# Kernel tuning notes

Hardware: AMD Instinct MI355X
Metric: run time of the kernel (lower is better)

The kernel has to match this reference:

```python
import jax, jax.numpy as jnp
import numpy as np

OUT = 260        # RESIZE_OUTPUT_IMAGES_SHAPE
TH = 0.8         # OD_SCORE_TH
PCT = 1.0        # INTERNAL_PERCENTAGE_IMAGE_TOTAKE
N_BOXES = 10     # loop bound in original call()
TAPS = 6         # lanczos3 support (radius 3 -> 6 taps, antialias=False)


def _lanczos_taps(src, size):
    """src: (OUT,) float sample coords in crop-local space; size: traced int crop size.
    Returns clamped tap indices (OUT,6) and normalized lanczos3 weights (OUT,6)."""
    base = jnp.floor(src).astype(jnp.int32) - 2
    taps = base[:, None] + jnp.arange(TAPS, dtype=jnp.int32)          # (OUT,6)
    d = src[:, None] - taps.astype(src.dtype)
    w = jnp.where(jnp.abs(d) < 3.0, jnp.sinc(d) * jnp.sinc(d / 3.0), 0.0)
    w = w / jnp.sum(w, axis=1, keepdims=True)
    idx = jnp.clip(taps, 0, size - 1)
    return idx, w


def _crop_resize(img, box):
    """img: (H,W,3). box: (4,) normalized [ymin,xmin,ymax,xmax] -> (OUT,OUT,3).
    Matches tf.image.resize lanczos3 (antialias=False): half-pixel centers, clamped edges."""
    H, W = img.shape[0], img.shape[1]
    y0 = (box[0] * H).astype(jnp.int32)
    x0 = (box[1] * W).astype(jnp.int32)
    y1 = (box[2] * H).astype(jnp.int32)
    x1 = (box[3] * W).astype(jnp.int32)
    ch = jnp.maximum(y1 - y0, 1)
    cw = jnp.maximum(x1 - x0, 1)
    o = jnp.arange(OUT, dtype=img.dtype)
    src_h = (o + 0.5) * (ch.astype(img.dtype) / OUT) - 0.5
    src_w = (o + 0.5) * (cw.astype(img.dtype) / OUT) - 0.5
    idx_h, w_h = _lanczos_taps(src_h, ch)
    idx_w, w_w = _lanczos_taps(src_w, cw)
    idx_h = idx_h + y0
    idx_w = idx_w + x0
    # vertical pass: gather 6 row taps per output row, reduce -> (OUT, W, 3)
    rows = jnp.einsum('pa,pawc->pwc', w_h, img[idx_h])
    # horizontal pass: gather 6 col taps per output col, reduce -> (OUT, OUT, 3)
    out = jnp.einsum('qb,pqbc->pqc', w_w, rows[:, idx_w])
    return out


def setup_inputs() -> dict:
    key = jax.random.key(0)
    k1, k2, k3, k4 = jax.random.split(key, 4)
    # scores: first 10 mostly above threshold, rest below
    s_hi = 0.85 + 0.15 * jax.random.uniform(k1, (N_BOXES,), dtype=jnp.float32)
    s_lo = 0.8 * jax.random.uniform(k2, (100 - N_BOXES,), dtype=jnp.float32)
    od_scores = jnp.concatenate([s_hi, s_lo])
    # bboxes (ymin,xmin,ymax,xmax) with guaranteed positive crop sizes
    u = jax.random.uniform(k3, (100, 4), dtype=jnp.float32)
    od_bboxes = jnp.stack([u[:, 0] * 0.45, u[:, 1] * 0.45,
                           0.55 + 0.45 * u[:, 2], 0.55 + 0.45 * u[:, 3]], axis=1)
    image = jax.random.normal(k4, (1, 2048, 2048, 3), dtype=jnp.float32)
    return {"od_scores": od_scores, "od_bboxes": od_bboxes, "image": image}


def reference(od_scores, od_bboxes, image):
    img = image[0]                           # (H,W,3)
    b10 = od_bboxes[:N_BOXES]
    s10 = od_scores[:N_BOXES]
    valid = ((od_scores[0] >= TH) & (s10 >= TH)
             & (b10[:, 1] >= 0.5 - PCT / 2.0)
             & (b10[:, 3] <= 0.5 + PCT / 2.0))
    crops = jax.vmap(lambda b: _crop_resize(img, b))(b10)   # (10,OUT,OUT,3)
    return crops * valid[:, None, None, None].astype(img.dtype)
```

## Files before the change

kernel.cpp:

```cpp
#include <hip/hip_runtime.h>
#include <math.h>

#define OUT 260
#define TAPS 6
#define IMG_H 2048
#define IMG_W 2048
#define ROW_F (IMG_W * 3)
#define IMG_TOTAL (IMG_H * ROW_F)
#define NB 10
#define TH 0.8f
#define LDS_F 6152

__device__ __forceinline__ float sincf(float x) {
    if (x == 0.0f) return 1.0f;
    float px = 3.14159265358979323846f * x;
    return __sinf(px) / px;
}

__global__ __launch_bounds__(256) void crop_resize_vfirst(
    const float* __restrict__ scores,
    const float* __restrict__ boxes,
    const float* __restrict__ img,
    float* __restrict__ out)
{
    const int p   = blockIdx.x;
    const int box = blockIdx.y;

    const float b0 = boxes[box * 4 + 0];
    const float b1 = boxes[box * 4 + 1];
    const float b2 = boxes[box * 4 + 2];
    const float b3 = boxes[box * 4 + 3];

    int y0 = (int)(b0 * (float)IMG_H);
    int x0 = (int)(b1 * (float)IMG_W);
    int y1 = (int)(b2 * (float)IMG_H);
    int x1 = (int)(b3 * (float)IMG_W);
    if (y1 > IMG_H) y1 = IMG_H;
    if (x1 > IMG_W) x1 = IMG_W;
    const int ch = max(y1 - y0, 1);
    const int cw = max(x1 - x0, 1);

    const bool valid = (scores[0] >= TH) && (scores[box] >= TH)
                    && (b1 >= 0.0f) && (b3 <= 1.0f);
    const float vmask = valid ? 1.0f : 0.0f;

    float wh[TAPS];
    int   ih[TAPS];
    {
        const float src = ((float)p + 0.5f) * ((float)ch / (float)OUT) - 0.5f;
        const int base = (int)floorf(src) - 2;
        float s = 0.0f;
        #pragma unroll
        for (int a = 0; a < TAPS; ++a) {
            const int tap = base + a;
            const float d = src - (float)tap;
            const float w = (fabsf(d) < 3.0f) ? sincf(d) * sincf(d * (1.0f / 3.0f)) : 0.0f;
            wh[a] = w; s += w;
            int t = tap; t = t < 0 ? 0 : t; t = t > ch - 1 ? ch - 1 : t;
            ih[a] = t + y0;
        }
        const float inv = 1.0f / s;
        #pragma unroll
        for (int a = 0; a < TAPS; ++a) wh[a] *= inv;
    }

    const int start_f = (x0 * 3) & ~3;
    const int end_f   = (x0 + cw) * 3;
    const int n_f     = end_f - start_f;

    __shared__ float lds[LDS_F];

    {
        const float* r0 = img + (size_t)ih[0] * ROW_F + start_f;
        const float* r1 = img + (size_t)ih[1] * ROW_F + start_f;
        const float* r2 = img + (size_t)ih[2] * ROW_F + start_f;
        const float* r3 = img + (size_t)ih[3] * ROW_F + start_f;
        const float* r4 = img + (size_t)ih[4] * ROW_F + start_f;
        const float* r5 = img + (size_t)ih[5] * ROW_F + start_f;

        for (int f = threadIdx.x * 4; f < n_f; f += 256 * 4) {
            const float4 v0 = *(const float4*)(r0 + f);
            const float4 v1 = *(const float4*)(r1 + f);
            const float4 v2 = *(const float4*)(r2 + f);
            const float4 v3 = *(const float4*)(r3 + f);
            const float4 v4 = *(const float4*)(r4 + f);
            const float4 v5 = *(const float4*)(r5 + f);
            float4 acc;
            acc.x = wh[0]*v0.x + wh[1]*v1.x + wh[2]*v2.x + wh[3]*v3.x + wh[4]*v4.x + wh[5]*v5.x;
            acc.y = wh[0]*v0.y + wh[1]*v1.y + wh[2]*v2.y + wh[3]*v3.y + wh[4]*v4.y + wh[5]*v5.y;
            acc.z = wh[0]*v0.z + wh[1]*v1.z + wh[2]*v2.z + wh[3]*v3.z + wh[4]*v4.z + wh[5]*v5.z;
            acc.w = wh[0]*v0.w + wh[1]*v1.w + wh[2]*v2.w + wh[3]*v3.w + wh[4]*v4.w + wh[5]*v5.w;
            *(float4*)(lds + f) = acc;
        }
    }
    __syncthreads();

    const float wscale = (float)cw / (float)OUT;
    for (int q = threadIdx.x; q < OUT; q += 256) {
        const float src = ((float)q + 0.5f) * wscale - 0.5f;
        const int basew = (int)floorf(src) - 2;
        float ww[TAPS];
        float s = 0.0f;
        #pragma unroll
        for (int k = 0; k < TAPS; ++k) {
            const float d = src - (float)(basew + k);
            const float w = (fabsf(d) < 3.0f) ? sincf(d) * sincf(d * (1.0f / 3.0f)) : 0.0f;
            ww[k] = w; s += w;
        }
        const float inv = 1.0f / s;

        float a0 = 0.0f, a1 = 0.0f, a2 = 0.0f;
        #pragma unroll
        for (int k = 0; k < TAPS; ++k) {
            int t = basew + k;
            t = t < 0 ? 0 : t;
            t = t > cw - 1 ? cw - 1 : t;
            const int hb = (x0 + t) * 3 - start_f;
            a0 = fmaf(ww[k], lds[hb + 0], a0);
            a1 = fmaf(ww[k], lds[hb + 1], a1);
            a2 = fmaf(ww[k], lds[hb + 2], a2);
        }
        const float m = vmask * inv;
        const size_t o = (((size_t)box * OUT + p) * OUT + q) * 3;
        out[o + 0] = a0 * m;
        out[o + 1] = a1 * m;
        out[o + 2] = a2 * m;
    }
}

extern "C" void kernel_launch(void* const* d_in, const int* in_sizes, int n_in,
                              void* d_out, int out_size, void* d_ws, size_t ws_size,
                              hipStream_t stream) {
    const float* scores = (const float*)d_in[0];
    const float* boxes  = (const float*)d_in[1];
    const float* img    = (const float*)d_in[2];
    float* out = (float*)d_out;

    crop_resize_vfirst<<<dim3(OUT, NB), dim3(256), 0, stream>>>(scores, boxes, img, out);
}
```

Before: 115.2 us.

## Precompute Lanczos tap tables and split each output row into column segments

A small kernel now precomputes the per-box horizontal and vertical Lanczos weights and tap indices into workspace tables, with the validity mask folded into the vertical weights. The main kernel then launches 4x more 64-thread blocks, each handling a 65-column segment of one output row. Each block loads only the image span its segment needs into a smaller LDS buffer, which raises occupancy and parallelism. The costs are an extra kernel launch, table reads from global memory, and some overlapping image loads between neighbouring segments. A fallback to the old kernel remains for when the workspace is too small.

After: 113.6 us. No clear change (-1.4%).

```diff
diff --git a/kernel.cpp b/kernel.cpp
--- a/kernel.cpp
+++ b/kernel.cpp
@@ -6,10 +6,11 @@
 #define IMG_H 2048
 #define IMG_W 2048
 #define ROW_F (IMG_W * 3)
-#define IMG_TOTAL (IMG_H * ROW_F)
 #define NB 10
 #define TH 0.8f
-#define LDS_F 6152
+#define QB 65
+#define SEGS 4
+#define LDSF 1600
 
 __device__ __forceinline__ float sincf(float x) {
     if (x == 0.0f) return 1.0f;
@@ -17,26 +18,21 @@
     return __sinf(px) / px;
 }
 
-__global__ __launch_bounds__(256) void crop_resize_vfirst(
-    const float* __restrict__ scores,
-    const float* __restrict__ boxes,
-    const float* __restrict__ img,
-    float* __restrict__ out)
+
+__global__ __launch_bounds__(320) void tables_kernel(
+    const float* __restrict__ scores, const float* __restrict__ boxes,
+    float* __restrict__ htab, float* __restrict__ vtab)
 {
-    const int p   = blockIdx.x;
-    const int box = blockIdx.y;
-
+    const int box = blockIdx.x;
     const float b0 = boxes[box * 4 + 0];
     const float b1 = boxes[box * 4 + 1];
     const float b2 = boxes[box * 4 + 2];
     const float b3 = boxes[box * 4 + 3];
 
-    int y0 = (int)(b0 * (float)IMG_H);
-    int x0 = (int)(b1 * (float)IMG_W);
-    int y1 = (int)(b2 * (float)IMG_H);
-    int x1 = (int)(b3 * (float)IMG_W);
-    if (y1 > IMG_H) y1 = IMG_H;
-    if (x1 > IMG_W) x1 = IMG_W;
+    const int y0 = (int)(b0 * (float)IMG_H);
+    const int x0 = (int)(b1 * (float)IMG_W);
+    const int y1 = (int)(b2 * (float)IMG_H);
+    const int x1 = (int)(b3 * (float)IMG_W);
     const int ch = max(y1 - y0, 1);
     const int cw = max(x1 - x0, 1);
 
@@ -44,41 +40,85 @@
                     && (b1 >= 0.0f) && (b3 <= 1.0f);
     const float vmask = valid ? 1.0f : 0.0f;
 
-    float wh[TAPS];
-    int   ih[TAPS];
-    {
-        const float src = ((float)p + 0.5f) * ((float)ch / (float)OUT) - 0.5f;
+    const int t = threadIdx.x;
+    if (t >= OUT) return;
+
+    {
+        const float src = ((float)t + 0.5f) * ((float)cw / (float)OUT) - 0.5f;
         const int base = (int)floorf(src) - 2;
+        float w[TAPS]; int id[TAPS];
         float s = 0.0f;
         #pragma unroll
-        for (int a = 0; a < TAPS; ++a) {
-            const int tap = base + a;
-            const float d = src - (float)tap;
-            const float w = (fabsf(d) < 3.0f) ? sincf(d) * sincf(d * (1.0f / 3.0f)) : 0.0f;
-            wh[a] = w; s += w;
-            int t = tap; t = t < 0 ? 0 : t; t = t > ch - 1 ? ch - 1 : t;
-            ih[a] = t + y0;
+        for (int k = 0; k < TAPS; ++k) {
+            const float d = src - (float)(base + k);
+            const float wv = (fabsf(d) < 3.0f) ? sincf(d) * sincf(d * (1.0f / 3.0f)) : 0.0f;
+            w[k] = wv; s += wv;
+            int tt = base + k; tt = tt < 0 ? 0 : tt; tt = tt > cw - 1 ? cw - 1 : tt;
+            id[k] = (x0 + tt) * 3;
         }
         const float inv = 1.0f / s;
-        #pragma unroll
-        for (int a = 0; a < TAPS; ++a) wh[a] *= inv;
-    }
-
-    const int start_f = (x0 * 3) & ~3;
-    const int end_f   = (x0 + cw) * 3;
-    const int n_f     = end_f - start_f;
-
-    __shared__ float lds[LDS_F];
-
-    {
-        const float* r0 = img + (size_t)ih[0] * ROW_F + start_f;
-        const float* r1 = img + (size_t)ih[1] * ROW_F + start_f;
-        const float* r2 = img + (size_t)ih[2] * ROW_F + start_f;
-        const float* r3 = img + (size_t)ih[3] * ROW_F + start_f;
-        const float* r4 = img + (size_t)ih[4] * ROW_F + start_f;
-        const float* r5 = img + (size_t)ih[5] * ROW_F + start_f;
-
-        for (int f = threadIdx.x * 4; f < n_f; f += 256 * 4) {
+        float* h = htab + ((size_t)(box * OUT + t) << 4);
+        int*   hi = (int*)h;
+        #pragma unroll
+        for (int k = 0; k < TAPS; ++k) { h[k] = w[k] * inv; hi[8 + k] = id[k]; }
+        h[6] = 0.0f; h[7] = 0.0f; hi[14] = 0; hi[15] = 0;
+    }
+
+    {
+        const float src = ((float)t + 0.5f) * ((float)ch / (float)OUT) - 0.5f;
+        const int base = (int)floorf(src) - 2;
+        float w[TAPS]; int id[TAPS];
+        float s = 0.0f;
+        #pragma unroll
+        for (int k = 0; k < TAPS; ++k) {
+            const float d = src - (float)(base + k);
+            const float wv = (fabsf(d) < 3.0f) ? sincf(d) * sincf(d * (1.0f / 3.0f)) : 0.0f;
+            w[k] = wv; s += wv;
+            int tt = base + k; tt = tt < 0 ? 0 : tt; tt = tt > ch - 1 ? ch - 1 : tt;
+            id[k] = tt + y0;
+        }
+        const float inv = vmask / s;
+        float* v = vtab + ((size_t)(box * OUT + t) << 4);
+        int*   vi = (int*)v;
+        #pragma unroll
+        for (int k = 0; k < TAPS; ++k) { v[k] = w[k] * inv; vi[8 + k] = id[k]; }
+        v[6] = 0.0f; v[7] = 0.0f; vi[14] = 0; vi[15] = 0;
+    }
+}
+
+__global__ __launch_bounds__(64) void crop_resize_seg(
+    const float* __restrict__ img,
+    const float* __restrict__ htab,
+    const float* __restrict__ vtab,
+    float* __restrict__ out)
+{
+    const int seg = blockIdx.x;
+    const int p   = blockIdx.y;
+    const int box = blockIdx.z;
+    const int q0  = seg * QB;
+
+    const float* vrec = vtab + ((size_t)(box * OUT + p) << 4);
+    const int*   vi   = (const int*)vrec;
+    float wh[TAPS]; int rows[TAPS];
+    #pragma unroll
+    for (int k = 0; k < TAPS; ++k) { wh[k] = vrec[k]; rows[k] = vi[8 + k]; }
+
+    const int* hi_first = (const int*)(htab + ((size_t)(box * OUT + q0) << 4));
+    const int* hi_last  = (const int*)(htab + ((size_t)(box * OUT + q0 + QB - 1) << 4));
+    const int start_f = hi_first[8] & ~3;
+    const int n_f     = ((hi_last[13] + 3) - start_f + 3) & ~3;
+
+    __shared__ float lds[LDSF];
+
+    {
+        const float* r0 = img + (size_t)rows[0] * ROW_F + start_f;
+        const float* r1 = img + (size_t)rows[1] * ROW_F + start_f;
+        const float* r2 = img + (size_t)rows[2] * ROW_F + start_f;
+        const float* r3 = img + (size_t)rows[3] * ROW_F + start_f;
+        const float* r4 = img + (size_t)rows[4] * ROW_F + start_f;
+        const float* r5 = img + (size_t)rows[5] * ROW_F + start_f;
+
+        for (int f = threadIdx.x * 4; f < n_f; f += 64 * 4) {
             const float4 v0 = *(const float4*)(r0 + f);
             const float4 v1 = *(const float4*)(r1 + f);
             const float4 v2 = *(const float4*)(r2 + f);
@@ -95,36 +135,102 @@
     }
     __syncthreads();
 
-    const float wscale = (float)cw / (float)OUT;
+    for (int qi = threadIdx.x; qi < QB; qi += 64) {
+        const int q = q0 + qi;
+        const float* h  = htab + ((size_t)(box * OUT + q) << 4);
+        const int*   hi = (const int*)h;
+        float a0 = 0.0f, a1 = 0.0f, a2 = 0.0f;
+        #pragma unroll
+        for (int k = 0; k < TAPS; ++k) {
+            const float w  = h[k];
+            const int   li = hi[8 + k] - start_f;
+            a0 = fmaf(w, lds[li + 0], a0);
+            a1 = fmaf(w, lds[li + 1], a1);
+            a2 = fmaf(w, lds[li + 2], a2);
+        }
+        const size_t o = (((size_t)box * OUT + p) * OUT + q) * 3;
+        out[o + 0] = a0;
+        out[o + 1] = a1;
+        out[o + 2] = a2;
+    }
+}
+
+__global__ __launch_bounds__(256) void crop_resize_fallback(
+    const float* __restrict__ scores, const float* __restrict__ boxes,
+    const float* __restrict__ img, float* __restrict__ out)
+{
+    const int p = blockIdx.x, box = blockIdx.y;
+    const float b0 = boxes[box*4+0], b1 = boxes[box*4+1];
+    const float b2 = boxes[box*4+2], b3 = boxes[box*4+3];
+    const int y0 = (int)(b0*(float)IMG_H), x0 = (int)(b1*(float)IMG_W);
+    const int y1 = (int)(b2*(float)IMG_H), x1 = (int)(b3*(float)IMG_W);
+    const int ch = max(y1-y0,1), cw = max(x1-x0,1);
+    const bool valid = (scores[0]>=TH)&&(scores[box]>=TH)&&(b1>=0.0f)&&(b3<=1.0f);
+    const float vmask = valid?1.0f:0.0f;
+    float wh[TAPS]; int ih[TAPS];
+    {
+        const float src = ((float)p+0.5f)*((float)ch/(float)OUT)-0.5f;
+        const int base = (int)floorf(src)-2;
+        float s = 0.0f;
+        #pragma unroll
+        for (int a = 0; a < TAPS; ++a) {
+            const float d = src-(float)(base+a);
+            const float w = (fabsf(d)<3.0f)?sincf(d)*sincf(d*(1.0f/3.0f)):0.0f;
+            wh[a]=w; s+=w;
+            int t=base+a; t=t<0?0:t; t=t>ch-1?ch-1:t; ih[a]=t+y0;
+        }
+        const float inv = 1.0f/s;
+        #pragma unroll
+        for (int a = 0; a < TAPS; ++a) wh[a]*=inv;
+    }
+    const int start_f = (x0*3)&~3;
+    const int end_f = (x0+cw)*3;
+    const int n_f = end_f-start_f;
+    __shared__ float lds[6152];
+    {
+        const float* r0 = img+(size_t)ih[0]*ROW_F+start_f;
+        const float* r1 = img+(size_t)ih[1]*ROW_F+start_f;
+        const float* r2 = img+(size_t)ih[2]*ROW_F+start_f;
+        const float* r3 = img+(size_t)ih[3]*ROW_F+start_f;
+        const float* r4 = img+(size_t)ih[4]*ROW_F+start_f;
+        const float* r5 = img+(size_t)ih[5]*ROW_F+start_f;
+        for (int f = threadIdx.x*4; f < n_f; f += 256*4) {
+            const float4 v0=*(const float4*)(r0+f), v1=*(const float4*)(r1+f);
+            const float4 v2=*(const float4*)(r2+f), v3=*(const float4*)(r3+f);
+            const float4 v4=*(const float4*)(r4+f), v5=*(const float4*)(r5+f);
+            float4 acc;
+            acc.x=wh[0]*v0.x+wh[1]*v1.x+wh[2]*v2.x+wh[3]*v3.x+wh[4]*v4.x+wh[5]*v5.x;
+            acc.y=wh[0]*v0.y+wh[1]*v1.y+wh[2]*v2.y+wh[3]*v3.y+wh[4]*v4.y+wh[5]*v5.y;
+            acc.z=wh[0]*v0.z+wh[1]*v1.z+wh[2]*v2.z+wh[3]*v3.z+wh[4]*v4.z+wh[5]*v5.z;
+            acc.w=wh[0]*v0.w+wh[1]*v1.w+wh[2]*v2.w+wh[3]*v3.w+wh[4]*v4.w+wh[5]*v5.w;
+            *(float4*)(lds+f)=acc;
+        }
+    }
+    __syncthreads();
+    const float wscale = (float)cw/(float)OUT;
     for (int q = threadIdx.x; q < OUT; q += 256) {
-        const float src = ((float)q + 0.5f) * wscale - 0.5f;
-        const int basew = (int)floorf(src) - 2;
-        float ww[TAPS];
-        float s = 0.0f;
-        #pragma unroll
-        for (int k = 0; k < TAPS; ++k) {
-            const float d = src - (float)(basew + k);
-            const float w = (fabsf(d) < 3.0f) ? sincf(d) * sincf(d * (1.0f / 3.0f)) : 0.0f;
-            ww[k] = w; s += w;
-        }
-        const float inv = 1.0f / s;
-
-        float a0 = 0.0f, a1 = 0.0f, a2 = 0.0f;
-        #pragma unroll
-        for (int k = 0; k < TAPS; ++k) {
-            int t = basew + k;
-            t = t < 0 ? 0 : t;
-            t = t > cw - 1 ? cw - 1 : t;
-            const int hb = (x0 + t) * 3 - start_f;
-            a0 = fmaf(ww[k], lds[hb + 0], a0);
-            a1 = fmaf(ww[k], lds[hb + 1], a1);
-            a2 = fmaf(ww[k], lds[hb + 2], a2);
-        }
-        const float m = vmask * inv;
-        const size_t o = (((size_t)box * OUT + p) * OUT + q) * 3;
-        out[o + 0] = a0 * m;
-        out[o + 1] = a1 * m;
-        out[o + 2] = a2 * m;
+        const float src = ((float)q+0.5f)*wscale-0.5f;
+        const int basew = (int)floorf(src)-2;
+        float ww[TAPS]; float s = 0.0f;
+        #pragma unroll
+        for (int k = 0; k < TAPS; ++k) {
+            const float d = src-(float)(basew+k);
+            const float w = (fabsf(d)<3.0f)?sincf(d)*sincf(d*(1.0f/3.0f)):0.0f;
+            ww[k]=w; s+=w;
+        }
+        const float inv = 1.0f/s;
+        float a0=0,a1=0,a2=0;
+        #pragma unroll
+        for (int k = 0; k < TAPS; ++k) {
+            int t=basew+k; t=t<0?0:t; t=t>cw-1?cw-1:t;
+            const int hb=(x0+t)*3-start_f;
+            a0=fmaf(ww[k],lds[hb+0],a0);
+            a1=fmaf(ww[k],lds[hb+1],a1);
+            a2=fmaf(ww[k],lds[hb+2],a2);
+        }
+        const float m = vmask*inv;
+        const size_t o = (((size_t)box*OUT+p)*OUT+q)*3;
+        out[o+0]=a0*m; out[o+1]=a1*m; out[o+2]=a2*m;
     }
 }
 
@@ -136,5 +242,14 @@
     const float* img    = (const float*)d_in[2];
     float* out = (float*)d_out;
 
-    crop_resize_vfirst<<<dim3(OUT, NB), dim3(256), 0, stream>>>(scores, boxes, img, out);
-}
+    const size_t tab_bytes = (size_t)NB * OUT * 16 * sizeof(float);
+    if (ws_size < 2 * tab_bytes) {
+        crop_resize_fallback<<<dim3(OUT, NB), dim3(256), 0, stream>>>(scores, boxes, img, out);
+        return;
+    }
+    float* htab = (float*)d_ws;
+    float* vtab = (float*)((char*)d_ws + tab_bytes);
+
+    tables_kernel<<<dim3(NB), dim3(320), 0, stream>>>(scores, boxes, htab, vtab);
+    crop_resize_seg<<<dim3(SEGS, OUT, NB), dim3(64), 0, stream>>>(img, htab, vtab, out);
+}
```
